# Performance work log

Hardware: AMD Instinct MI355X
Metric: run time of the kernel (lower is better)

## Reference

```python
import jax, jax.numpy as jnp
import numpy as np

K = 10  # neighbors (k = min(k, N-1); N=4096 >> 10)
EPS = 1e-5  # InstanceNorm eps (torch default)


def knn_idx(coords, k):
    # coords: [B,3,N] -> indices of k nearest neighbors (excluding self) [B,N,k]
    pts = coords.transpose(0, 2, 1)  # [B,N,3]
    sq = jnp.sum(pts * pts, axis=-1)  # [B,N]
    dist = sq[:, :, None] + sq[:, None, :] - 2.0 * jnp.einsum('bnc,bmc->bnm', pts, pts)
    dist = jnp.clip(dist, 1e-12)
    _, idx = jax.lax.top_k(-dist, k + 1)  # ascending distance, sorted
    return idx[:, :, 1:]  # drop self


def graph_feature(idx, feats):
    # feats: [B,C,N], idx: [B,N,k] -> [B,2C,N,k] = [center, neighbor-center]
    neigh = jax.vmap(lambda f, i: f[:, i])(feats, idx)  # [B,C,N,k]
    center = jnp.broadcast_to(feats[..., None], neigh.shape)
    return jnp.concatenate([center, neigh - center], axis=1)


def instance_norm(x):
    # x: [B,C,N,k]; normalize over spatial dims per (batch, channel), no affine
    mu = jnp.mean(x, axis=(2, 3), keepdims=True)
    var = jnp.var(x, axis=(2, 3), keepdims=True)
    return (x - mu) * jax.lax.rsqrt(var + EPS)


def lrelu(x):
    return jnp.where(x >= 0, x, 0.2 * x)


def setup_inputs() -> dict:
    key = jax.random.key(0)
    k1, k2, k3, k4, k5 = jax.random.split(key, 5)
    B, C, N = 4, 128, 4096
    coords = jax.random.normal(k1, (B, 3, N), dtype=jnp.float32)
    features = jax.random.normal(k2, (B, C, N), dtype=jnp.float32)
    W1 = jax.random.normal(k3, (C, 2 * C), dtype=jnp.float32) * 0.05
    W2 = jax.random.normal(k4, (2 * C, 2 * C), dtype=jnp.float32) * 0.05
    W3 = jax.random.normal(k5, (C, 4 * C), dtype=jnp.float32) * 0.05
    return {"coords": coords, "features": features, "W1": W1, "W2": W2, "W3": W3}


def reference(coords, features, W1, W2, W3):
    idx = knn_idx(coords, K)  # same KNN graph used by both EdgeConv stages
    x0 = features  # [B,C,N]
    # stage 1: EdgeConv C -> C
    g1 = graph_feature(idx, x0)  # [B,2C,N,k]
    x1 = lrelu(instance_norm(jnp.einsum('oc,bcnk->bonk', W1, g1)))
    x1 = jnp.max(x1, axis=-1)  # [B,C,N]
    # stage 2: EdgeConv C -> 2C
    g2 = graph_feature(idx, x1)  # [B,2C,N,k] (input C, cat -> 2C)
    x2 = lrelu(instance_norm(jnp.einsum('oc,bcnk->bonk', W2, g2)))
    x2 = jnp.max(x2, axis=-1)  # [B,2C,N]
    # fuse: [x0,x1,x2] -> 4C -> C via conv1x1 + InstanceNorm (spatial = N)
    x3 = jnp.concatenate([x0, x1, x2], axis=1)  # [B,4C,N]
    x3 = jnp.einsum('oc,bcn->bon', W3, x3)[..., None]  # [B,C,N,1]
    x3 = lrelu(instance_norm(x3))[..., 0]  # [B,C,N]
    return x3
```

## Files before the change

### kernel.cpp

```cpp
#include <hip/hip_runtime.h>
#include <math.h>
#include <stdint.h>

#define NB 4
#define NC 128
#define NP 4096
#define KNN 10


__device__ __forceinline__ uint16_t f2bf(float f) {
  uint32_t u = __float_as_uint(f);
  u += 0x7fffu + ((u >> 16) & 1u);
  return (uint16_t)(u >> 16);
}

__device__ __forceinline__ void async16(const void* g, void* l) {
  __builtin_amdgcn_global_load_lds(
      (const __attribute__((address_space(1))) unsigned int*)g,
      (__attribute__((address_space(3))) unsigned int*)l,
      16, 0, 0);
}

__device__ __forceinline__ uint32_t fsort(float f) {
  uint32_t u = __float_as_uint(f);
  return (u & 0x80000000u) ? ~u : (u | 0x80000000u);
}
__device__ __forceinline__ float funsort(uint32_t k) {
  uint32_t u = (k & 0x80000000u) ? (k & 0x7fffffffu) : ~k;
  return __uint_as_float(u);
}

typedef __bf16 bf16x8 __attribute__((ext_vector_type(8)));
typedef float f32x4 __attribute__((ext_vector_type(4)));

__global__ void k_prep(const float* __restrict__ W1, const float* __restrict__ W2,
                       const float* __restrict__ W3, const float* __restrict__ coords,
                       uint16_t* __restrict__ W1cat, uint16_t* __restrict__ W2cat,
                       uint16_t* __restrict__ W3b,
                       float* __restrict__ stats, float4* __restrict__ pts4) {
  int t = blockIdx.x * 256 + threadIdx.x;
  if (t < 32768) {
    int o = t >> 7, c = t & 127;
    float v;
    if (o < 128) v = W1[o * 256 + c] - W1[o * 256 + 128 + c];
    else         v = W1[(o - 128) * 256 + 128 + c];
    W1cat[t] = f2bf(v);
  } else if (t < 98304) {
    int t2 = t - 32768;
    int o = t2 >> 7, c = t2 & 127;
    float v;
    if (o < 256) v = W2[o * 256 + c] - W2[o * 256 + 128 + c];
    else         v = W2[(o - 256) * 256 + 128 + c];
    W2cat[t2] = f2bf(v);
  } else if (t < 163840) {
    int t2 = t - 98304;
    W3b[t2] = f2bf(W3[t2]);
  } else if (t < 163840 + 8192) {
    stats[t - 163840] = 0.f;
  } else if (t < 163840 + 8192 + 16384) {
    int t2 = t - 163840 - 8192;
    int b = t2 >> 12, n = t2 & 4095;
    const float* cb = coords + b * 12288;
    float x = cb[n], y = cb[4096 + n], z = cb[8192 + n];
    float w = fmaf(x, x, fmaf(y, y, z * z));
    pts4[t2] = make_float4(x, y, z, w);
  }
}

__global__ void k_trans_feat(const float* __restrict__ feat, uint16_t* __restrict__ Xcat) {
  __shared__ float tile[32][33];
  int bid = blockIdx.x;
  int b = bid >> 9;
  int r = bid & 511;
  int n0 = (r >> 2) << 5;
  int c0 = (r & 3) << 5;
  int tx = threadIdx.x & 31, ty = threadIdx.x >> 5;
#pragma unroll
  for (int i = 0; i < 4; i++) {
    int c = c0 + ty + i * 8;
    tile[ty + i * 8][tx] = feat[(b * 128 + c) * 4096 + n0 + tx];
  }
  __syncthreads();
#pragma unroll
  for (int i = 0; i < 4; i++) {
    int n = n0 + ty + i * 8;
    Xcat[((b * 4096 + n) * 512) + c0 + tx] = f2bf(tile[tx][ty + i * 8]);
  }
}

__global__ void k_knn_thr(const float4* __restrict__ pts4, float* __restrict__ candd) {
  int L = blockIdx.x;
  int ch = L & 7;
  int qb = (L >> 3) & 15;
  int b = L >> 7;
  int m0 = ch << 7;
  const float4* pb = pts4 + b * 4096;
  int t = threadIdx.x;
  int q = (qb << 8) + t;
  float4 qp = pb[q];
  float d10[10];
#pragma unroll
  for (int i = 0; i < 10; i++) d10[i] = 1e30f;
#pragma unroll 2
  for (int mm = 0; mm < 128; mm++) {
    int m = m0 + mm;
    float4 p = pb[m];
    float dot = fmaf(qp.x, p.x, fmaf(qp.y, p.y, qp.z * p.z));
    float s = qp.w + p.w;
    float d = fmaf(-2.f, dot, s);
    d = (m == q) ? 1e30f : d;
    if (d < d10[9]) {
      float carry = d;
#pragma unroll
      for (int i = 0; i < 10; i++) {
        float lo = fminf(d10[i], carry);
        carry = fmaxf(d10[i], carry);
        d10[i] = lo;
      }
    }
  }
  int row = b * 4096 + q;
#pragma unroll
  for (int i = 0; i < 10; i++) candd[row * 80 + ch * 10 + i] = d10[i];
}

__global__ void k_knn_merge(const float* __restrict__ candd, float* __restrict__ tq) {
  int gw = blockIdx.x * 4 + (threadIdx.x >> 6);
  int l = threadIdx.x & 63;
  const float* cp = candd + (size_t)gw * 80;
  uint32_t k0 = fsort(cp[l]);
  uint32_t k1 = (l < 16) ? fsort(cp[64 + l]) : 0xFFFFFFFFu;
  uint32_t g = 0;
#pragma unroll
  for (int it = 0; it < 10; it++) {
    uint32_t m = k0 < k1 ? k0 : k1;
#pragma unroll
    for (int s = 1; s < 64; s <<= 1) {
      uint32_t o = __shfl_xor(m, s);
      m = o < m ? o : m;
    }
    g = m;
    if (it < 9) {
      if (k0 == m) k0 = 0xFFFFFFFFu;
      else if (k1 == m) k1 = 0xFFFFFFFFu;
    }
  }
  if (l == 0) tq[gw] = funsort(g);
}

#define CFCAP 128
__global__ __launch_bounds__(256) void k_knn_cf(
    const float4* __restrict__ pts4, const float* __restrict__ tq,
    int* __restrict__ idxout) {
  __shared__ float4 sp[2][544];
  __shared__ unsigned long long cand[8 * CFCAP];
  __shared__ int ccnt[8];
  int blk = blockIdx.x;
  int b = blk >> 9;
  int qg = blk & 511;
  int t = threadIdx.x;
  int ql = t & 7;
  int sub = t >> 3;
  if (t < 8) ccnt[t] = 0;
  const float4* pb = pts4 + b * 4096;
  int q = qg * 8 + ql;
  float4 qp = pb[q];
  float thr = tq[b * 4096 + q];
  int s0 = (t >> 4) * 17 + (t & 15);
  int s1 = s0 + 272;
  sp[0][s0] = pb[t];
  sp[0][s1] = pb[256 + t];
  __syncthreads();
  for (int c = 0; c < 8; c++) {
    int cur = c & 1;
    float4 w0, w1;
    if (c < 7) {
      w0 = pb[(c + 1) * 512 + t];
      w1 = pb[(c + 1) * 512 + 256 + t];
    }
    int base = sub * 17;
    int mb = c * 512 + sub * 16;
#pragma unroll
    for (int i = 0; i < 16; i++) {
      float4 p = sp[cur][base + i];
      int m = mb + i;
      float dot = fmaf(qp.x, p.x, fmaf(qp.y, p.y, qp.z * p.z));
      float s = qp.w + p.w;
      float d = fmaf(-2.f, dot, s);
      d = (m == q) ? 1e30f : d;
      if (d <= thr) {
        int pos = atomicAdd(&ccnt[ql], 1);
        if (pos < CFCAP)
          cand[ql * CFCAP + pos] = (((unsigned long long)fsort(d)) << 32) | (uint32_t)m;
      }
    }
    if (c < 7) {
      sp[cur ^ 1][s0] = w0;
      sp[cur ^ 1][s1] = w1;
    }
    __syncthreads();
  }
  int w = t >> 6;
  int l = t & 63;
  for (int k = 0; k < 2; k++) {
    int ql2 = w * 2 + k;
    int c = ccnt[ql2]; c = c < CFCAP ? c : CFCAP;
    unsigned long long k0 = (l < c) ? cand[ql2 * CFCAP + l] : ~0ULL;
    unsigned long long k1 = (64 + l < c) ? cand[ql2 * CFCAP + 64 + l] : ~0ULL;
    uint32_t keep[10];
#pragma unroll
    for (int it = 0; it < 10; it++) {
      unsigned long long m = k0 < k1 ? k0 : k1;
#pragma unroll
      for (int s = 1; s < 64; s <<= 1) {
        unsigned long long o = __shfl_xor(m, s);
        m = o < m ? o : m;
      }
      keep[it] = (uint32_t)(m & 0xffffffffu);
      if (k0 == m) k0 = ~0ULL;
      else if (k1 == m) k1 = ~0ULL;
    }
    if (l == 0) {
      int orow = b * 4096 + qg * 8 + ql2;
#pragma unroll
      for (int i = 0; i < 10; i++) idxout[orow * 10 + i] = (int)keep[i];
    }
  }
}

__global__ __launch_bounds__(256) void k_gemm_bf(
    const uint16_t* __restrict__ Xb, int ldx, int xoff,
    const uint16_t* __restrict__ Wb, int ldw,
    float* __restrict__ Y, int ldy, int K) {
  __shared__ __align__(16) uint8_t lds[49152];
  const int t = threadIdx.x;
  const int l = t & 63;
  const int wid = t >> 6;
  const int wr = wid & 1, wc = wid >> 1;
  const int p0 = blockIdx.x * 128;
  const int o0 = blockIdx.y * 64;

  const int rA = l >> 3;
  const int cbp = ((l & 7) ^ rA) << 4;
  const int swl = (l & 7) << 4;

  f32x4 acc[4][2];
#pragma unroll
  for (int mi = 0; mi < 4; mi++)
#pragma unroll
    for (int ni = 0; ni < 2; ni++) acc[mi][ni] = (f32x4)0.f;

  auto stage = [&](int k0, int buf) {
    const uint16_t* Xs_ = Xb + (size_t)p0 * ldx + xoff + k0;
    const uint16_t* Ws_ = Wb + (size_t)o0 * ldw + k0;
#pragma unroll
    for (int cc = 0; cc < 4; cc++) {
      int c = wid * 4 + cc;
      const uint8_t* g = (const uint8_t*)(Xs_ + (size_t)(c * 8 + rA) * ldx) + cbp;
      async16(g, &lds[buf * 16384 + c * 1024]);
    }
#pragma unroll
    for (int cc = 0; cc < 2; cc++) {
      int c = wid * 2 + cc;
      const uint8_t* g = (const uint8_t*)(Ws_ + (size_t)(c * 8 + rA) * ldw) + cbp;
      async16(g, &lds[32768 + buf * 8192 + c * 1024]);
    }
  };

  auto compute = [&](int buf) {
    const uint8_t* Ab = &lds[buf * 16384];
    const uint8_t* Bb = &lds[32768 + buf * 8192];
#pragma unroll
    for (int ks = 0; ks < 2; ks++) {
      int cb = ks * 64 + ((l >> 4) << 4);
      bf16x8 bfr[2];
#pragma unroll
      for (int ni = 0; ni < 2; ni++) {
        int n = wc * 32 + ni * 16 + (l & 15);
        bfr[ni] = *(const bf16x8*)(Bb + n * 128 + (cb ^ swl));
      }
#pragma unroll
      for (int mi = 0; mi < 4; mi++) {
        int m = wr * 64 + mi * 16 + (l & 15);
        bf16x8 afr = *(const bf16x8*)(Ab + m * 128 + (cb ^ swl));
        acc[mi][0] = __builtin_amdgcn_mfma_f32_16x16x32_bf16(afr, bfr[0], acc[mi][0], 0, 0, 0);
        acc[mi][1] = __builtin_amdgcn_mfma_f32_16x16x32_bf16(afr, bfr[1], acc[mi][1], 0, 0, 0);
      }
    }
  };

  const int nsteps = K >> 6;
  stage(0, 0);
  for (int s = 0; s < nsteps; s++) {
    __syncthreads();
    if (s + 1 < nsteps) stage((s + 1) << 6, (s + 1) & 1);
    compute(s & 1);
  }

#pragma unroll
  for (int mi = 0; mi < 4; mi++)
#pragma unroll
    for (int ni = 0; ni < 2; ni++) {
      int col = o0 + wc * 32 + ni * 16 + (l & 15);
      int row0 = p0 + wr * 64 + mi * 16 + (l >> 4) * 4;
#pragma unroll
      for (int j = 0; j < 4; j++)
        Y[(size_t)(row0 + j) * ldy + col] = acc[mi][ni][j];
    }
}

template <int O>
__global__ void k_gather(const float* __restrict__ UV, int ld, int voff,
                         const int* __restrict__ idx,
                         float* __restrict__ M,
                         float* __restrict__ T1, float* __restrict__ T2) {
  int L = blockIdx.x;
  int rx = L & 7;
  int b = rx >> 1;
  int j = ((L >> 3) << 1) + (rx & 1);
  int n0 = j << 4;
  int o = threadIdx.x;
  float a1 = 0.f, a2 = 0.f;
  for (int pi = 0; pi < 16; pi++) {
    int row = b * 4096 + n0 + pi;
    float u = UV[row * ld + o];
    float s1 = 0.f, s2 = 0.f, vmax = -1e30f;
#pragma unroll
    for (int jj = 0; jj < KNN; jj++) {
      int m = idx[row * 10 + jj];
      float v = UV[(b * 4096 + m) * ld + voff + o];
      s1 += v;
      float x = u + v;
      s2 = fmaf(x, x, s2);
      vmax = fmaxf(vmax, v);
    }
    M[row * O + o] = vmax;
    a1 += 10.f * u + s1;
    a2 += s2;
  }
  atomicAdd(&T1[b * O + o], a1);
  atomicAdd(&T2[b * O + o], a2);
}

template <int O>
__global__ void k_passB(const float* __restrict__ UV, int ld,
                        const float* __restrict__ M, int coff,
                        const float* __restrict__ T1, const float* __restrict__ T2,
                        uint16_t* __restrict__ Xcat) {
  int t = blockIdx.x * 256 + threadIdx.x;
  int o = t & (O - 1);
  int pn = t / O;
  int b = pn >> 12;
  float mu = T1[b * O + o] * (1.f / 40960.f);
  float e2 = T2[b * O + o] * (1.f / 40960.f);
  float inv = rsqrtf(e2 - mu * mu + 1e-5f);
  float x = (UV[pn * ld + o] + M[pn * O + o] - mu) * inv;
  Xcat[pn * 512 + coff + o] = f2bf(x >= 0.f ? x : 0.2f * x);
}

__global__ void k_stats3(const float* __restrict__ Y3, float* __restrict__ T1, float* __restrict__ T2) {
  int L = blockIdx.x;
  int rx = L & 7;
  int b = rx >> 1;
  int j = ((L >> 3) << 1) + (rx & 1);
  int n0 = j << 4;
  int o = threadIdx.x;
  float a1 = 0.f, a2 = 0.f;
  for (int pi = 0; pi < 16; pi++) {
    float y = Y3[(b * 4096 + n0 + pi) * 128 + o];
    a1 += y;
    a2 = fmaf(y, y, a2);
  }
  atomicAdd(&T1[b * 128 + o], a1);
  atomicAdd(&T2[b * 128 + o], a2);
}

__global__ void k_out(const float* __restrict__ Y3, const float* __restrict__ T1,
                      const float* __restrict__ T2, float* __restrict__ out) {
  __shared__ float tile[32][33];
  int bid = blockIdx.x;
  int b = bid >> 9;
  int r = bid & 511;
  int n0 = (r >> 2) << 5;
  int o0 = (r & 3) << 5;
  int tx = threadIdx.x & 31, ty = threadIdx.x >> 5;
  int o = o0 + tx;
  float mu = T1[b * 128 + o] * (1.f / 4096.f);
  float e2 = T2[b * 128 + o] * (1.f / 4096.f);
  float inv = rsqrtf(e2 - mu * mu + 1e-5f);
#pragma unroll
  for (int i = 0; i < 4; i++) {
    int n = n0 + ty + i * 8;
    float v = (Y3[(b * 4096 + n) * 128 + o] - mu) * inv;
    tile[ty + i * 8][tx] = v >= 0.f ? v : 0.2f * v;
  }
  __syncthreads();
#pragma unroll
  for (int i = 0; i < 4; i++) {
    int oo = o0 + ty + i * 8;
    out[(b * 128 + oo) * 4096 + n0 + tx] = tile[tx][ty + i * 8];
  }
}

extern "C" void kernel_launch(void* const* d_in, const int* in_sizes, int n_in,
                              void* d_out, int out_size, void* d_ws, size_t ws_size,
                              hipStream_t stream) {
  const float* coords   = (const float*)d_in[0];
  const float* features = (const float*)d_in[1];
  const float* W1       = (const float*)d_in[2];
  const float* W2       = (const float*)d_in[3];
  const float* W3       = (const float*)d_in[4];
  float* out = (float*)d_out;

  float*    ws    = (float*)d_ws;
  uint16_t* Xcat  = (uint16_t*)ws;
  float*    UV    = ws + 4194304;
  float*    Mbuf  = ws + 12582912;
  float*    Y3    = Mbuf;
  int*      idxb  = (int*)(ws + 16777216);
  uint16_t* W1cat = (uint16_t*)(ws + 16941056);
  uint16_t* W2cat = (uint16_t*)(ws + 16957440);
  uint16_t* W3b   = (uint16_t*)(ws + 16990208);
  float*    stats = ws + 17022976;
  float*  candd = UV;
  float*  tq    = UV + 1310720;
  float4* pts4  = (float4*)(UV + 1327104);

  k_prep<<<736, 256, 0, stream>>>(W1, W2, W3, coords, W1cat, W2cat, W3b, stats, pts4);
  k_trans_feat<<<2048, 256, 0, stream>>>(features, Xcat);
  k_knn_thr<<<512, 256, 0, stream>>>(pts4, candd);
  k_knn_merge<<<4096, 256, 0, stream>>>(candd, tq);
  k_knn_cf<<<2048, 256, 0, stream>>>(pts4, tq, idxb);

  k_gemm_bf<<<dim3(128, 4), 256, 0, stream>>>(Xcat, 512, 0, W1cat, 128, UV, 256, 128);
  k_gather<128><<<1024, 128, 0, stream>>>(UV, 256, 128, idxb, Mbuf, stats + 0, stats + 512);
  k_passB<128><<<8192, 256, 0, stream>>>(UV, 256, Mbuf, 128, stats + 0, stats + 512, Xcat);

  k_gemm_bf<<<dim3(128, 8), 256, 0, stream>>>(Xcat, 512, 128, W2cat, 128, UV, 512, 128);
  k_gather<256><<<1024, 256, 0, stream>>>(UV, 512, 256, idxb, Mbuf, stats + 1024, stats + 2048);
  k_passB<256><<<16384, 256, 0, stream>>>(UV, 512, Mbuf, 256, stats + 1024, stats + 2048, Xcat);

  k_gemm_bf<<<dim3(128, 2), 256, 0, stream>>>(Xcat, 512, 0, W3b, 512, Y3, 128, 512);
  k_stats3<<<1024, 128, 0, stream>>>(Y3, stats + 3072, stats + 3584);
  k_out<<<2048, 256, 0, stream>>>(Y3, stats + 3072, stats + 3584, out);
}
```

Before: 192.1 us.

## Slim KNN candidate filter and recompute exact distances only for survivors

The candidate-filter KNN kernel now tests a cheaper rearranged expression (-2q·p + |p|^2 against threshold minus |q|^2 plus a margin) and stores only candidate indices. Exact distances and sort keys are recomputed in the selection phase for the survivors, reading points from global memory. The double-buffered LDS staging is replaced by a single buffer with two barriers per chunk, and the candidate capacity grows to 160 with a third key register per lane. The margin keeps near-threshold points from being dropped because of rounding, but it also admits more candidates, and the single buffer gives up overlap of loads with compute.

```diff
diff --git a/kernel.cpp b/kernel.cpp
--- a/kernel.cpp
+++ b/kernel.cpp
@@ -148,12 +148,13 @@
   if (l == 0) tq[gw] = funsort(g);
 }
 
-#define CFCAP 128
+#define CFCAP 160
+#define DMARGIN 1e-3f
 __global__ __launch_bounds__(256) void k_knn_cf(
     const float4* __restrict__ pts4, const float* __restrict__ tq,
     int* __restrict__ idxout) {
-  __shared__ float4 sp[2][544];
-  __shared__ unsigned long long cand[8 * CFCAP];
+  __shared__ float4 sp[544];
+  __shared__ int candi[8 * CFCAP];
   __shared__ int ccnt[8];
   int blk = blockIdx.x;
   int b = blk >> 9;
@@ -165,52 +166,55 @@
   const float4* pb = pts4 + b * 4096;
   int q = qg * 8 + ql;
   float4 qp = pb[q];
-  float thr = tq[b * 4096 + q];
+  float q2x = -2.f * qp.x, q2y = -2.f * qp.y, q2z = -2.f * qp.z;
+  float rhs = tq[b * 4096 + q] + DMARGIN - qp.w;
   int s0 = (t >> 4) * 17 + (t & 15);
   int s1 = s0 + 272;
-  sp[0][s0] = pb[t];
-  sp[0][s1] = pb[256 + t];
-  __syncthreads();
   for (int c = 0; c < 8; c++) {
-    int cur = c & 1;
-    float4 w0, w1;
-    if (c < 7) {
-      w0 = pb[(c + 1) * 512 + t];
-      w1 = pb[(c + 1) * 512 + 256 + t];
-    }
+    __syncthreads();
+    sp[s0] = pb[c * 512 + t];
+    sp[s1] = pb[c * 512 + 256 + t];
+    __syncthreads();
     int base = sub * 17;
     int mb = c * 512 + sub * 16;
 #pragma unroll
     for (int i = 0; i < 16; i++) {
-      float4 p = sp[cur][base + i];
-      int m = mb + i;
-      float dot = fmaf(qp.x, p.x, fmaf(qp.y, p.y, qp.z * p.z));
-      float s = qp.w + p.w;
-      float d = fmaf(-2.f, dot, s);
-      d = (m == q) ? 1e30f : d;
-      if (d <= thr) {
+      float4 p = sp[base + i];
+      float tt = fmaf(q2x, p.x, fmaf(q2y, p.y, fmaf(q2z, p.z, p.w)));
+      if (tt <= rhs) {
         int pos = atomicAdd(&ccnt[ql], 1);
-        if (pos < CFCAP)
-          cand[ql * CFCAP + pos] = (((unsigned long long)fsort(d)) << 32) | (uint32_t)m;
-      }
-    }
-    if (c < 7) {
-      sp[cur ^ 1][s0] = w0;
-      sp[cur ^ 1][s1] = w1;
-    }
-    __syncthreads();
-  }
+        if (pos < CFCAP) candi[ql * CFCAP + pos] = mb + i;
+      }
+    }
+  }
+  __syncthreads();
   int w = t >> 6;
   int l = t & 63;
   for (int k = 0; k < 2; k++) {
     int ql2 = w * 2 + k;
+    int q2 = qg * 8 + ql2;
+    float4 qp2 = pb[q2];
     int c = ccnt[ql2]; c = c < CFCAP ? c : CFCAP;
-    unsigned long long k0 = (l < c) ? cand[ql2 * CFCAP + l] : ~0ULL;
-    unsigned long long k1 = (64 + l < c) ? cand[ql2 * CFCAP + 64 + l] : ~0ULL;
+    unsigned long long k0 = ~0ULL, k1 = ~0ULL, k2 = ~0ULL;
+#pragma unroll
+    for (int u = 0; u < 3; u++) {
+      int j = u * 64 + l;
+      if (j < c) {
+        int m = candi[ql2 * CFCAP + j];
+        float4 p = pb[m];
+        float dot = fmaf(qp2.x, p.x, fmaf(qp2.y, p.y, qp2.z * p.z));
+        float s = qp2.w + p.w;
+        float d = fmaf(-2.f, dot, s);
+        d = (m == q2) ? 1e30f : d;
+        unsigned long long key = (((unsigned long long)fsort(d)) << 32) | (uint32_t)m;
+        if (u == 0) k0 = key; else if (u == 1) k1 = key; else k2 = key;
+      }
+    }
     uint32_t keep[10];
 #pragma unroll
     for (int it = 0; it < 10; it++) {
       unsigned long long m = k0 < k1 ? k0 : k1;
+      m = k2 < m ? k2 : m;
 #pragma unroll
       for (int s = 1; s < 64; s <<= 1) {
         unsigned long long o = __shfl_xor(m, s);
@@ -219,9 +223,10 @@
       keep[it] = (uint32_t)(m & 0xffffffffu);
       if (k0 == m) k0 = ~0ULL;
       else if (k1 == m) k1 = ~0ULL;
+      else if (k2 == m) k2 = ~0ULL;
     }
     if (l == 0) {
-      int orow = b * 4096 + qg * 8 + ql2;
+      int orow = b * 4096 + q2;
 #pragma unroll
       for (int i = 0; i < 10; i++) idxout[orow * 10 + i] = (int)keep[i];
     }
```

Result: faster. 182.6 us (-4.9%).
